# Optimization experiments

Hardware: AMD Instinct MI355X
Metric: run time of the kernel (lower is better)

Reference implementation:

```python
import jax, jax.numpy as jnp
import numpy as np

N_NODES = 50000
NNZ = 1250000
N_EDGES = 1600000
VOCAB = 40000
HIDDEN = 128
LABELS = 2000
NUM_GCN = 2


def setup_inputs() -> dict:
    key = jax.random.key(0)
    ks = jax.random.split(key, 16)
    feat_ids = jax.random.randint(ks[0], (NNZ,), 0, VOCAB, dtype=jnp.int32)
    mid = jnp.sort(jax.random.randint(ks[1], (N_NODES - 1,), 0, NNZ, dtype=jnp.int32))
    offsets = jnp.concatenate([jnp.zeros((1,), jnp.int32), mid, jnp.full((1,), NNZ, jnp.int32)])
    feat_weights = jax.random.uniform(ks[2], (NNZ,), jnp.float32)
    edge_src = jax.random.randint(ks[3], (N_EDGES,), 0, N_NODES, dtype=jnp.int32)
    edge_dst = jax.random.randint(ks[4], (N_EDGES,), 0, N_NODES, dtype=jnp.int32)
    ppi_w = jax.random.uniform(ks[5], (N_EDGES,), jnp.float32)
    self_w = jax.random.uniform(ks[6], (N_EDGES,), jnp.float32)
    # learned params (xavier-ish scaling)
    emb_weight = jax.random.normal(ks[7], (VOCAB, HIDDEN), jnp.float32) * 0.02
    input_bias = jnp.zeros((HIDDEN,), jnp.float32)
    W1 = jax.random.normal(ks[8], (HIDDEN, HIDDEN), jnp.float32) * (1.0 / np.sqrt(HIDDEN))
    b1 = jnp.zeros((HIDDEN,), jnp.float32)
    W2 = jax.random.normal(ks[9], (HIDDEN, HIDDEN), jnp.float32) * (1.0 / np.sqrt(HIDDEN))
    b2 = jnp.zeros((HIDDEN,), jnp.float32)
    Wo = jax.random.normal(ks[10], (HIDDEN, LABELS), jnp.float32) * (1.0 / np.sqrt(HIDDEN))
    bo = jnp.zeros((LABELS,), jnp.float32)
    return {
        'feat_ids': feat_ids, 'offsets': offsets, 'feat_weights': feat_weights,
        'edge_src': edge_src, 'edge_dst': edge_dst, 'ppi_w': ppi_w, 'self_w': self_w,
        'emb_weight': emb_weight, 'input_bias': input_bias,
        'W1': W1, 'b1': b1, 'W2': W2, 'b2': b2, 'Wo': Wo, 'bo': bo,
    }


def _embedding_bag_sum(emb_weight, feat_ids, offsets, feat_weights):
    # EmbeddingBag(mode='sum', include_last_offset=True) with per_sample_weights:
    # bag b sums feat_weights[i] * emb_weight[feat_ids[i]] for i in [offsets[b], offsets[b+1]).
    bag_id = jnp.searchsorted(offsets, jnp.arange(NNZ, dtype=offsets.dtype), side='right') - 1
    vals = emb_weight[feat_ids] * feat_weights[:, None]  # [NNZ, H]
    return jax.ops.segment_sum(vals, bag_id, num_segments=N_NODES)  # [N, H]


def reference(feat_ids, offsets, feat_weights, edge_src, edge_dst, ppi_w, self_w,
              emb_weight, input_bias, W1, b1, W2, b2, Wo, bo):
    # input layer: EmbeddingBag sum + bias -> relu (dropout = identity in eval)
    h = jax.nn.relu(_embedding_bag_sum(emb_weight, feat_ids, offsets, feat_weights) + input_bias)
    for (W, b) in ((W1, b1), (W2, b2)):
        hs = h[edge_src]                                            # gather [E, H]
        res = jax.ops.segment_sum(hs * self_w[:, None], edge_dst, num_segments=N_NODES)
        agg = jax.ops.segment_sum(hs * ppi_w[:, None], edge_dst, num_segments=N_NODES)
        # NodeUpdate: dropout(relu(Linear(ppi_out))) + res  (dropout identity)
        h = jax.nn.relu(agg @ W + b) + res
    return h @ Wo + bo  # [N, LABELS]
```

## Files before the change

### kernel.cpp

```cpp
#include <hip/hip_runtime.h>

#define HID 128

typedef __bf16 bf16x8 __attribute__((ext_vector_type(8)));
typedef float f32x4 __attribute__((ext_vector_type(4)));

__device__ __forceinline__ unsigned short f2bf(float x) {
  unsigned int u = __builtin_bit_cast(unsigned int, x);
  u += 0x7FFFu + ((u >> 16) & 1u);
  return (unsigned short)(u >> 16);
}
__device__ __forceinline__ float bf2f(unsigned short x) {
  return __builtin_bit_cast(float, (unsigned int)x << 16);
}

__global__ void zero_int_kernel(int* __restrict__ p, int n) {
  int i = blockIdx.x * blockDim.x + threadIdx.x;
  if (i < n) p[i] = 0;
}

__global__ void degree_kernel(const int* __restrict__ dst, int* __restrict__ deg, int n) {
  int i = blockIdx.x * blockDim.x + threadIdx.x;
  if (i < n) atomicAdd(&deg[dst[i]], 1);
}

__global__ void __launch_bounds__(1024) scan_kernel(const int* __restrict__ deg,
                                                    int* __restrict__ eoff, int n) {
  __shared__ int ssum[1024];
  int t = threadIdx.x;
  int chunk = (n + 1023) / 1024;
  int beg = t * chunk;
  int end = min(beg + chunk, n);
  int s = 0;
  for (int i = beg; i < end; ++i) s += deg[i];
  ssum[t] = s;
  __syncthreads();
  for (int off = 1; off < 1024; off <<= 1) {
    int v = (t >= off) ? ssum[t - off] : 0;
    __syncthreads();
    ssum[t] += v;
    __syncthreads();
  }
  int base = (t == 0) ? 0 : ssum[t - 1];
  for (int i = beg; i < end; ++i) { eoff[i] = base; base += deg[i]; }
  if (t == 1023) eoff[n] = base;
}

__global__ void copy_int_kernel(const int* __restrict__ src, int* __restrict__ dst, int n) {
  int i = blockIdx.x * blockDim.x + threadIdx.x;
  if (i < n) dst[i] = src[i];
}

__global__ void scatter_kernel(const int* __restrict__ edst, const int* __restrict__ esrc,
                               const float* __restrict__ ppi, const float* __restrict__ selfw,
                               int* __restrict__ cursor, int4* __restrict__ edges, int n) {
  int i = blockIdx.x * blockDim.x + threadIdx.x;
  if (i < n) {
    int d = edst[i];
    int pos = atomicAdd(&cursor[d], 1);
    edges[pos] = make_int4(esrc[i], __builtin_bit_cast(int, ppi[i]),
                           __builtin_bit_cast(int, selfw[i]), 0);
  }
}

__global__ void cast_emb_kernel(const float* __restrict__ emb,
                                unsigned short* __restrict__ embb, int n) {
  int i = blockIdx.x * blockDim.x + threadIdx.x;
  if (i < n) embb[i] = f2bf(emb[i]);
}

__global__ void __launch_bounds__(256) embed_kernel(const int* __restrict__ ids,
                                                    const int* __restrict__ offs,
                                                    const float* __restrict__ fw,
                                                    const unsigned int* __restrict__ embb,
                                                    const float* __restrict__ bias,
                                                    unsigned int* __restrict__ hb, int n_nodes) {
  int node = blockIdx.x * 4 + (threadIdx.x >> 6);
  if (node >= n_nodes) return;
  int u = threadIdx.x & 63;
  int beg = offs[node], end = offs[node + 1];
  float a0 = 0.f, a1 = 0.f;
  int i = beg;
  for (; i + 8 <= end; i += 8) {
    int id[8];
    float w[8];
    unsigned int v[8];
#pragma unroll
    for (int q = 0; q < 8; ++q) id[q] = ids[i + q];
#pragma unroll
    for (int q = 0; q < 8; ++q) w[q] = fw[i + q];
#pragma unroll
    for (int q = 0; q < 8; ++q) v[q] = embb[(long)id[q] * 64 + u];
#pragma unroll
    for (int q = 0; q < 8; ++q) {
      a0 += w[q] * bf2f((unsigned short)(v[q] & 0xffffu));
      a1 += w[q] * bf2f((unsigned short)(v[q] >> 16));
    }
  }
  for (; i < end; ++i) {
    unsigned int v = embb[(long)ids[i] * 64 + u];
    float w = fw[i];
    a0 += w * bf2f((unsigned short)(v & 0xffffu));
    a1 += w * bf2f((unsigned short)(v >> 16));
  }
  a0 += bias[2 * u];
  a1 += bias[2 * u + 1];
  a0 = a0 > 0.f ? a0 : 0.f;
  a1 = a1 > 0.f ? a1 : 0.f;
  hb[(long)node * 64 + u] = (unsigned int)f2bf(a0) | ((unsigned int)f2bf(a1) << 16);
}

__global__ void __launch_bounds__(256) aggregate_kernel(const unsigned int* __restrict__ hb,
                                                        const int* __restrict__ eoff,
                                                        const int4* __restrict__ edges,
                                                        float2* __restrict__ agg,
                                                        float2* __restrict__ res, int n_nodes) {
  int node = blockIdx.x * 4 + (threadIdx.x >> 6);
  if (node >= n_nodes) return;
  int u = threadIdx.x & 63;
  int beg = eoff[node], end = eoff[node + 1];
  float a0 = 0.f, a1 = 0.f, r0 = 0.f, r1 = 0.f;
  int j = beg;
  for (; j + 8 <= end; j += 8) {
    int4 e[8];
    unsigned int v[8];
#pragma unroll
    for (int q = 0; q < 8; ++q) e[q] = edges[j + q];
#pragma unroll
    for (int q = 0; q < 8; ++q) v[q] = hb[(long)e[q].x * 64 + u];
#pragma unroll
    for (int q = 0; q < 8; ++q) {
      float lo = bf2f((unsigned short)(v[q] & 0xffffu));
      float hi = bf2f((unsigned short)(v[q] >> 16));
      float wp = __builtin_bit_cast(float, e[q].y);
      float ws = __builtin_bit_cast(float, e[q].z);
      a0 += wp * lo; a1 += wp * hi;
      r0 += ws * lo; r1 += ws * hi;
    }
  }
  for (; j < end; ++j) {
    int4 e = edges[j];
    unsigned int v = hb[(long)e.x * 64 + u];
    float lo = bf2f((unsigned short)(v & 0xffffu));
    float hi = bf2f((unsigned short)(v >> 16));
    float wp = __builtin_bit_cast(float, e.y);
    float ws = __builtin_bit_cast(float, e.z);
    a0 += wp * lo; a1 += wp * hi;
    r0 += ws * lo; r1 += ws * hi;
  }
  agg[(long)node * 64 + u] = make_float2(a0, a1);
  res[(long)node * 64 + u] = make_float2(r0, r1);
}

__global__ void __launch_bounds__(256) update_kernel(const float* __restrict__ agg,
                                                     const float* __restrict__ res,
                                                     const float* __restrict__ W,
                                                     const float* __restrict__ b,
                                                     unsigned short* __restrict__ hout,
                                                     int n_nodes) {
  __shared__ __align__(16) float sW[HID * HID];
  __shared__ float sx[2][HID];
  int t = threadIdx.x & (HID - 1);
  int sub = threadIdx.x >> 7;
  for (int i = threadIdx.x; i < HID * HID / 4; i += 256)
    ((float4*)sW)[i] = ((const float4*)W)[i];
  float bias = b[t];
  __syncthreads();
  for (int node0 = blockIdx.x * 2; node0 < n_nodes; node0 += gridDim.x * 2) {
    int node = node0 + sub;
    bool valid = node < n_nodes;
    if (valid) sx[sub][t] = agg[(long)node * HID + t];
    __syncthreads();
    if (valid) {
      float acc = 0.f;
#pragma unroll 16
      for (int k = 0; k < HID; ++k) acc += sx[sub][k] * sW[k * HID + t];
      float v = acc + bias;
      v = v > 0.f ? v : 0.f;
      hout[(long)node * HID + t] = f2bf(v + res[(long)node * HID + t]);
    }
    __syncthreads();
  }
}

__global__ void transpose_wo_kernel(const float* __restrict__ Wo,
                                    unsigned short* __restrict__ WoT, int labels) {
  int idx = blockIdx.x * 256 + threadIdx.x;
  if (idx < labels * HID) {
    int n = idx >> 7, k = idx & (HID - 1);
    WoT[idx] = f2bf(Wo[(long)k * labels + n]);
  }
}

#define LDK 136

__global__ void __launch_bounds__(256) out_gemm_kernel(const unsigned short* __restrict__ hb,
                                                       const unsigned short* __restrict__ WoT,
                                                       const float* __restrict__ bo,
                                                       float* __restrict__ out,
                                                       int n_nodes, int labels) {
  __shared__ __align__(16) unsigned short sA[64 * LDK];
  __shared__ __align__(16) unsigned short sB[80 * LDK];
  int m0 = blockIdx.x * 64;
  int n0 = blockIdx.y * 80;
  int tid = threadIdx.x;

  for (int i = tid; i < 64 * 32; i += 256) {
    int r = i >> 5, c4 = i & 31;
    int row = m0 + r;
    if (row >= n_nodes) row = n_nodes - 1;
    ushort4 v = ((const ushort4*)(hb + (long)row * HID))[c4];
    *(ushort4*)&sA[r * LDK + c4 * 4] = v;
  }
  for (int i = tid; i < 80 * 32; i += 256) {
    int r = i >> 5, c4 = i & 31;
    ushort4 v = ((const ushort4*)(WoT + (long)(n0 + r) * HID))[c4];
    *(ushort4*)&sB[r * LDK + c4 * 4] = v;
  }
  __syncthreads();

  int wave = tid >> 6, lane = tid & 63;
  int lrow = lane & 15, quad = lane >> 4;
  f32x4 acc[5];
#pragma unroll
  for (int c = 0; c < 5; ++c) acc[c] = (f32x4){0.f, 0.f, 0.f, 0.f};

#pragma unroll
  for (int kk = 0; kk < 4; ++kk) {
    bf16x8 af = *(const bf16x8*)&sA[(wave * 16 + lrow) * LDK + kk * 32 + quad * 8];
#pragma unroll
    for (int c = 0; c < 5; ++c) {
      bf16x8 bf = *(const bf16x8*)&sB[(c * 16 + lrow) * LDK + kk * 32 + quad * 8];
      acc[c] = __builtin_amdgcn_mfma_f32_16x16x32_bf16(af, bf, acc[c], 0, 0, 0);
    }
  }

#pragma unroll
  for (int c = 0; c < 5; ++c) {
    int n = n0 + c * 16 + lrow;
    float bias = bo[n];
#pragma unroll
    for (int r = 0; r < 4; ++r) {
      int m = m0 + wave * 16 + quad * 4 + r;
      if (m < n_nodes) out[(long)m * labels + n] = acc[c][r] + bias;
    }
  }
}

extern "C" void kernel_launch(void* const* d_in, const int* in_sizes, int n_in,
                              void* d_out, int out_size, void* d_ws, size_t ws_size,
                              hipStream_t stream) {
  const int* feat_ids = (const int*)d_in[0];
  const int* offsets = (const int*)d_in[1];
  const float* feat_w = (const float*)d_in[2];
  const int* esrc = (const int*)d_in[3];
  const int* edst = (const int*)d_in[4];
  const float* ppi = (const float*)d_in[5];
  const float* selfw = (const float*)d_in[6];
  const float* emb = (const float*)d_in[7];
  const float* ibias = (const float*)d_in[8];
  const float* W1 = (const float*)d_in[9];
  const float* b1 = (const float*)d_in[10];
  const float* W2 = (const float*)d_in[11];
  const float* b2 = (const float*)d_in[12];
  const float* Wo = (const float*)d_in[13];
  const float* bo = (const float*)d_in[14];
  float* out = (float*)d_out;

  int N = in_sizes[1] - 1;
  int E = in_sizes[3];
  int EMBN = in_sizes[7];
  int LABELS = in_sizes[14];

  char* ws = (char*)d_ws;
  size_t HN = (size_t)N * HID;
  unsigned short* h_bf = (unsigned short*)ws;  ws += HN * 2;
  float* agg = (float*)ws;                     ws += HN * 4;
  float* res = (float*)ws;                     ws += HN * 4;
  unsigned short* WoT = (unsigned short*)ws;   ws += (size_t)LABELS * HID * 2;
  unsigned short* embb = (unsigned short*)ws;  ws += (size_t)EMBN * 2;
  int4* edges = (int4*)ws;                     ws += (size_t)E * 16;
  int* deg = (int*)ws;                         ws += (size_t)N * 4;
  int* eoff = (int*)ws;                        ws += (size_t)(N + 1) * 4;
  int* cursor = (int*)ws;                      ws += (size_t)N * 4;

  zero_int_kernel<<<(N + 255) / 256, 256, 0, stream>>>(deg, N);
  degree_kernel<<<(E + 255) / 256, 256, 0, stream>>>(edst, deg, E);
  scan_kernel<<<1, 1024, 0, stream>>>(deg, eoff, N);
  copy_int_kernel<<<(N + 255) / 256, 256, 0, stream>>>(eoff, cursor, N);
  scatter_kernel<<<(E + 255) / 256, 256, 0, stream>>>(edst, esrc, ppi, selfw,
                                                      cursor, edges, E);

  cast_emb_kernel<<<(EMBN + 255) / 256, 256, 0, stream>>>(emb, embb, EMBN);
  embed_kernel<<<(N + 3) / 4, 256, 0, stream>>>(feat_ids, offsets, feat_w,
                                                (const unsigned int*)embb, ibias,
                                                (unsigned int*)h_bf, N);
  transpose_wo_kernel<<<(LABELS * HID + 255) / 256, 256, 0, stream>>>(Wo, WoT, LABELS);

  aggregate_kernel<<<(N + 3) / 4, 256, 0, stream>>>((const unsigned int*)h_bf, eoff, edges,
                                                    (float2*)agg, (float2*)res, N);
  update_kernel<<<1024, 256, 0, stream>>>(agg, res, W1, b1, h_bf, N);
  aggregate_kernel<<<(N + 3) / 4, 256, 0, stream>>>((const unsigned int*)h_bf, eoff, edges,
                                                    (float2*)agg, (float2*)res, N);
  update_kernel<<<1024, 256, 0, stream>>>(agg, res, W2, b2, h_bf, N);

  dim3 g((N + 63) / 64, LABELS / 80);
  out_gemm_kernel<<<g, 256, 0, stream>>>(h_bf, WoT, bo, out, N, LABELS);
}
```

Before: 1.281 ms.

## Split embed and aggregate gathers into feature slices with 4 rows per wave

The embedding-bag and neighbour-aggregation kernels now launch a second grid dimension of 4 feature slices. Each wavefront splits into 4 groups of 16 lanes, each group gathering a different edge or feature row, and partial sums are combined with cross-lane shuffles. The aim is more independent gathers in flight per wave and more waves overall, at the cost of re-reading offsets and edge records once per slice and using 64-byte gather segments instead of 256-byte ones.

Result: slower. 1.387 ms (+8.2%).

```diff
diff --git a/kernel.cpp b/kernel.cpp
--- a/kernel.cpp
+++ b/kernel.cpp
@@ -77,37 +77,52 @@
                                                     unsigned int* __restrict__ hb, int n_nodes) {
   int node = blockIdx.x * 4 + (threadIdx.x >> 6);
   if (node >= n_nodes) return;
-  int u = threadIdx.x & 63;
+  int slice = blockIdx.y;
+  int u = threadIdx.x & 63, g = u >> 4, c = u & 15;
   int beg = offs[node], end = offs[node + 1];
+  const unsigned int* es = embb + slice * 16 + c;
   float a0 = 0.f, a1 = 0.f;
   int i = beg;
-  for (; i + 8 <= end; i += 8) {
+  for (; i + 32 <= end; i += 32) {
     int id[8];
     float w[8];
     unsigned int v[8];
 #pragma unroll
-    for (int q = 0; q < 8; ++q) id[q] = ids[i + q];
-#pragma unroll
-    for (int q = 0; q < 8; ++q) w[q] = fw[i + q];
-#pragma unroll
-    for (int q = 0; q < 8; ++q) v[q] = embb[(long)id[q] * 64 + u];
+    for (int q = 0; q < 8; ++q) id[q] = ids[i + 4 * q + g];
+#pragma unroll
+    for (int q = 0; q < 8; ++q) w[q] = fw[i + 4 * q + g];
+#pragma unroll
+    for (int q = 0; q < 8; ++q) v[q] = es[(long)id[q] * 64];
 #pragma unroll
     for (int q = 0; q < 8; ++q) {
       a0 += w[q] * bf2f((unsigned short)(v[q] & 0xffffu));
       a1 += w[q] * bf2f((unsigned short)(v[q] >> 16));
     }
   }
-  for (; i < end; ++i) {
-    unsigned int v = embb[(long)ids[i] * 64 + u];
-    float w = fw[i];
+  for (; i + 8 <= end; i += 8) {
+    int id0 = ids[i + g], id1 = ids[i + 4 + g];
+    float w0 = fw[i + g], w1 = fw[i + 4 + g];
+    unsigned int v0 = es[(long)id0 * 64];
+    unsigned int v1 = es[(long)id1 * 64];
+    a0 += w0 * bf2f((unsigned short)(v0 & 0xffffu)) + w1 * bf2f((unsigned short)(v1 & 0xffffu));
+    a1 += w0 * bf2f((unsigned short)(v0 >> 16)) + w1 * bf2f((unsigned short)(v1 >> 16));
+  }
+  for (int it = i + g; it < end; it += 4) {
+    int id = ids[it];
+    float w = fw[it];
+    unsigned int v = es[(long)id * 64];
     a0 += w * bf2f((unsigned short)(v & 0xffffu));
     a1 += w * bf2f((unsigned short)(v >> 16));
   }
-  a0 += bias[2 * u];
-  a1 += bias[2 * u + 1];
-  a0 = a0 > 0.f ? a0 : 0.f;
-  a1 = a1 > 0.f ? a1 : 0.f;
-  hb[(long)node * 64 + u] = (unsigned int)f2bf(a0) | ((unsigned int)f2bf(a1) << 16);
+  a0 += __shfl_xor(a0, 16); a1 += __shfl_xor(a1, 16);
+  a0 += __shfl_xor(a0, 32); a1 += __shfl_xor(a1, 32);
+  if (u < 16) {
+    float x0 = a0 + bias[slice * 32 + 2 * u];
+    float x1 = a1 + bias[slice * 32 + 2 * u + 1];
+    x0 = x0 > 0.f ? x0 : 0.f;
+    x1 = x1 > 0.f ? x1 : 0.f;
+    hb[(long)node * 64 + slice * 16 + u] = (unsigned int)f2bf(x0) | ((unsigned int)f2bf(x1) << 16);
+  }
 }
 
 __global__ void __launch_bounds__(256) aggregate_kernel(const unsigned int* __restrict__ hb,
@@ -117,17 +132,19 @@
                                                         float2* __restrict__ res, int n_nodes) {
   int node = blockIdx.x * 4 + (threadIdx.x >> 6);
   if (node >= n_nodes) return;
-  int u = threadIdx.x & 63;
+  int slice = blockIdx.y;
+  int u = threadIdx.x & 63, g = u >> 4, c = u & 15;
   int beg = eoff[node], end = eoff[node + 1];
+  const unsigned int* hs = hb + slice * 16 + c;
   float a0 = 0.f, a1 = 0.f, r0 = 0.f, r1 = 0.f;
   int j = beg;
-  for (; j + 8 <= end; j += 8) {
+  for (; j + 32 <= end; j += 32) {
     int4 e[8];
     unsigned int v[8];
 #pragma unroll
-    for (int q = 0; q < 8; ++q) e[q] = edges[j + q];
-#pragma unroll
-    for (int q = 0; q < 8; ++q) v[q] = hb[(long)e[q].x * 64 + u];
+    for (int q = 0; q < 8; ++q) e[q] = edges[j + 4 * q + g];
+#pragma unroll
+    for (int q = 0; q < 8; ++q) v[q] = hs[(long)e[q].x * 64];
 #pragma unroll
     for (int q = 0; q < 8; ++q) {
       float lo = bf2f((unsigned short)(v[q] & 0xffffu));
@@ -138,9 +155,23 @@
       r0 += ws * lo; r1 += ws * hi;
     }
   }
-  for (; j < end; ++j) {
-    int4 e = edges[j];
-    unsigned int v = hb[(long)e.x * 64 + u];
+  for (; j + 8 <= end; j += 8) {
+    int4 e0 = edges[j + g];
+    int4 e1 = edges[j + 4 + g];
+    unsigned int v0 = hs[(long)e0.x * 64];
+    unsigned int v1 = hs[(long)e1.x * 64];
+    float lo0 = bf2f((unsigned short)(v0 & 0xffffu)), hi0 = bf2f((unsigned short)(v0 >> 16));
+    float lo1 = bf2f((unsigned short)(v1 & 0xffffu)), hi1 = bf2f((unsigned short)(v1 >> 16));
+    float wp0 = __builtin_bit_cast(float, e0.y), ws0 = __builtin_bit_cast(float, e0.z);
+    float wp1 = __builtin_bit_cast(float, e1.y), ws1 = __builtin_bit_cast(float, e1.z);
+    a0 += wp0 * lo0 + wp1 * lo1;
+    a1 += wp0 * hi0 + wp1 * hi1;
+    r0 += ws0 * lo0 + ws1 * lo1;
+    r1 += ws0 * hi0 + ws1 * hi1;
+  }
+  for (int jt = j + g; jt < end; jt += 4) {
+    int4 e = edges[jt];
+    unsigned int v = hs[(long)e.x * 64];
     float lo = bf2f((unsigned short)(v & 0xffffu));
     float hi = bf2f((unsigned short)(v >> 16));
     float wp = __builtin_bit_cast(float, e.y);
@@ -148,8 +179,15 @@
     a0 += wp * lo; a1 += wp * hi;
     r0 += ws * lo; r1 += ws * hi;
   }
-  agg[(long)node * 64 + u] = make_float2(a0, a1);
-  res[(long)node * 64 + u] = make_float2(r0, r1);
+  a0 += __shfl_xor(a0, 16); a1 += __shfl_xor(a1, 16);
+  r0 += __shfl_xor(r0, 16); r1 += __shfl_xor(r1, 16);
+  a0 += __shfl_xor(a0, 32); a1 += __shfl_xor(a1, 32);
+  r0 += __shfl_xor(r0, 32); r1 += __shfl_xor(r1, 32);
+  if (u < 16) {
+    long idx = (long)node * 64 + slice * 16 + u;
+    agg[idx] = make_float2(a0, a1);
+    res[idx] = make_float2(r0, r1);
+  }
 }
 
 __global__ void __launch_bounds__(256) update_kernel(const float* __restrict__ agg,
@@ -292,16 +330,17 @@
                                                       cursor, edges, E);
 
   cast_emb_kernel<<<(EMBN + 255) / 256, 256, 0, stream>>>(emb, embb, EMBN);
-  embed_kernel<<<(N + 3) / 4, 256, 0, stream>>>(feat_ids, offsets, feat_w,
-                                                (const unsigned int*)embb, ibias,
-                                                (unsigned int*)h_bf, N);
+  dim3 gs((N + 3) / 4, 4);
+  embed_kernel<<<gs, 256, 0, stream>>>(feat_ids, offsets, feat_w,
+                                       (const unsigned int*)embb, ibias,
+                                       (unsigned int*)h_bf, N);
   transpose_wo_kernel<<<(LABELS * HID + 255) / 256, 256, 0, stream>>>(Wo, WoT, LABELS);
 
-  aggregate_kernel<<<(N + 3) / 4, 256, 0, stream>>>((const unsigned int*)h_bf, eoff, edges,
-                                                    (float2*)agg, (float2*)res, N);
+  aggregate_kernel<<<gs, 256, 0, stream>>>((const unsigned int*)h_bf, eoff, edges,
+                                           (float2*)agg, (float2*)res, N);
   update_kernel<<<1024, 256, 0, stream>>>(agg, res, W1, b1, h_bf, N);
-  aggregate_kernel<<<(N + 3) / 4, 256, 0, stream>>>((const unsigned int*)h_bf, eoff, edges,
-                                                    (float2*)agg, (float2*)res, N);
+  aggregate_kernel<<<gs, 256, 0, stream>>>((const unsigned int*)h_bf, eoff, edges,
+                                           (float2*)agg, (float2*)res, N);
   update_kernel<<<1024, 256, 0, stream>>>(agg, res, W2, b2, h_bf, N);
 
   dim3 g((N + 63) / 64, LABELS / 80);
```
